# Kernel tuning notes

Measured on AMD Instinct MI355X. Metric: run time of the kernel, lower is better.

The kernel has to match this reference:

```python
import jax, jax.numpy as jnp
import numpy as np

N = 50000      # nodes
E = 800000     # edges
F = 32         # num_features (per-irrep channels, L=1 -> scalar + vector parts)
NINV = 128     # num_inv_features
NL = 4         # num_layers
H = 64         # edge-MLP hidden width (mlp_params)
G = 2048       # number of graphs
EPS = 1e-6


def setup_inputs() -> dict:
    key = jax.random.key(0)
    ks = jax.random.split(key, 24)
    inp = {
        "x": jax.random.normal(ks[0], (N, 5), jnp.float32),
        "pos": jax.random.normal(ks[1], (N, 3), jnp.float32),
        "edge_index": jax.random.randint(ks[2], (2, E), 0, N, jnp.int64),
        "edge_attr": jax.random.uniform(ks[3], (E, 4), jnp.float32),
        "batch": jnp.sort(jax.random.randint(ks[4], (N,), 0, G, jnp.int64)),
        # embedding block params (scalar and vector branches)
        "W_es": jax.random.normal(ks[5], (5, F), jnp.float32) * 0.3,
        "b_es": jnp.zeros((F,), jnp.float32),
        "W_ev": jax.random.normal(ks[6], (5, F), jnp.float32) * 0.3,
        # per-layer message-passing params, stacked over layers
        "W1": jax.random.normal(ks[7], (NL, 5, H), jnp.float32) * 0.3,
        "b1": jnp.zeros((NL, H), jnp.float32),
        "W2": jax.random.normal(ks[8], (NL, H, 3 * F), jnp.float32) * 0.1,
        "b2": jnp.zeros((NL, 3 * F), jnp.float32),
        "Ws": jax.random.normal(ks[9], (NL, F, F), jnp.float32) * 0.1,
        "Wv": jax.random.normal(ks[10], (NL, F, F), jnp.float32) * 0.1,
        # invariant map
        "W_inv": jax.random.normal(ks[11], (2 * F, NINV), jnp.float32) * 0.1,
        "b_inv": jnp.zeros((NINV,), jnp.float32),
        # fc head: BN -> ELU -> Linear -> BN -> ELU -> Linear(->1)
        "g1": jnp.ones((NINV,), jnp.float32),
        "be1": jnp.zeros((NINV,), jnp.float32),
        "Wf1": jax.random.normal(ks[12], (NINV, NINV), jnp.float32) * 0.1,
        "bf1": jnp.zeros((NINV,), jnp.float32),
        "g2": jnp.ones((NINV,), jnp.float32),
        "be2": jnp.zeros((NINV,), jnp.float32),
        "Wf2": jax.random.normal(ks[13], (NINV, 1), jnp.float32) * 0.1,
        "bf2": jnp.zeros((1,), jnp.float32),
    }
    return inp


def _bn(z, g, b):
    m = z.mean(0)
    va = z.var(0)
    return (z - m) * jax.lax.rsqrt(va + 1e-5) * g + b


def reference(x, pos, edge_index, edge_attr, batch,
              W_es, b_es, W_ev, W1, b1, W2, b2, Ws, Wv,
              W_inv, b_inv, g1, be1, Wf1, bf1, g2, be2, Wf2, bf2):
    src, dst = edge_index[0], edge_index[1]
    delta = pos[dst] - pos[src]                       # [E,3]
    d = jnp.sqrt(jnp.sum(delta * delta, -1) + EPS)    # [E]
    u = delta / d[:, None]                            # unit edge direction

    # embedding: L=1 steerable features = scalar [N,F] + vector [N,F,3]
    s = x @ W_es + b_es
    v = (x @ W_ev)[:, :, None] * pos[:, None, :]

    edge_in = jnp.concatenate([d[:, None], edge_attr], -1)   # [E,5]
    counts = jax.ops.segment_sum(jnp.ones((E,), s.dtype), dst, num_segments=N)
    denom = jnp.maximum(counts, 1.0)[:, None]

    for l in range(NL):  # residual message-passing blocks
        h = jax.nn.elu(edge_in @ W1[l] + b1[l]) @ W2[l] + b2[l]  # [E,3F]
        gs, gv, gsv = jnp.split(h, 3, axis=-1)
        ms = gs * s[src]                                          # [E,F]
        mv = gv[:, :, None] * v[src] + (gsv * s[src])[:, :, None] * u[:, None, :]  # [E,F,3]
        as_ = jax.ops.segment_sum(ms, dst, num_segments=N) / denom
        av = jax.ops.segment_sum(mv, dst, num_segments=N) / denom[:, :, None]
        s = s + jax.nn.elu(as_ @ Ws[l])
        v = v + jnp.einsum('nfd,fg->ngd', av, Wv[l])

    # invariant map: scalars + vector norms
    inv_feats = jnp.concatenate([s, jnp.sqrt(jnp.sum(v * v, -1) + EPS)], -1)
    inv = inv_feats @ W_inv + b_inv                               # [N,NINV]

    # global mean pool over graphs
    gcnt = jnp.maximum(jax.ops.segment_sum(jnp.ones((N,), inv.dtype), batch, num_segments=G), 1.0)[:, None]
    xg = jax.ops.segment_sum(inv, batch, num_segments=G) / gcnt   # [G,NINV]

    z = jax.nn.elu(_bn(xg, g1, be1)) @ Wf1 + bf1
    z = jax.nn.elu(_bn(z, g2, be2)) @ Wf2 + bf2                   # [G,1]
    return z
```

## Files before the change

kernel.cpp:

```cpp
#include <hip/hip_runtime.h>
#include <hip/hip_bf16.h>
#include <math.h>

#define NN 50000
#define EE 800000
#define FF 32
#define HH 64
#define GG 2048
#define NLAYERS 4
#define EPSF 1e-6f
#define TILES 4

typedef __attribute__((ext_vector_type(8))) short short8;
typedef __attribute__((ext_vector_type(4))) float f32x4;

__device__ __forceinline__ float elu_f(float x){ return x > 0.0f ? x : __expf(x) - 1.0f; }
__device__ __forceinline__ short f2bf_s(float x){
    __hip_bfloat16 h = __float2bfloat16(x);
    return *reinterpret_cast<short*>(&h);
}
__device__ __forceinline__ float bf2f(unsigned short u){
    unsigned int w = ((unsigned int)u) << 16;
    return *reinterpret_cast<float*>(&w);
}

__global__ __launch_bounds__(256) void k_count(const int* __restrict__ ei, int* __restrict__ counts)
{
    int e = blockIdx.x*256 + threadIdx.x;
    if (e >= EE) return;
    atomicAdd(&counts[ei[EE+e]], 1);
}

__global__ __launch_bounds__(1024) void k_scan(const int* __restrict__ counts, int* __restrict__ rowptr)
{
    __shared__ int sh[1024];
    const int CH = (NN + 1023)/1024;
    int t = threadIdx.x;
    int start = t*CH;
    int end = min(start+CH, NN);
    int s = 0;
    for (int i=start; i<end; i++) s += counts[i];
    sh[t] = s; __syncthreads();
    for (int off=1; off<1024; off<<=1){
        int v = (t>=off) ? sh[t-off] : 0;
        __syncthreads();
        sh[t] += v;
        __syncthreads();
    }
    int run = sh[t] - s;
    for (int i=start; i<end; i++){ rowptr[i] = run; run += counts[i]; }
    if (t==1023) rowptr[NN] = run;
}

__global__ __launch_bounds__(256) void k_fill(
    const int* __restrict__ ei, const float* __restrict__ pos, const float* __restrict__ eattr,
    const int* __restrict__ rowptr, int* __restrict__ cursor,
    int* __restrict__ esrc, float* __restrict__ ein8)
{
    int e = blockIdx.x*256 + threadIdx.x;
    if (e >= EE) return;
    int src = ei[e], dst = ei[EE+e];
    float dx = pos[dst*3+0]-pos[src*3+0];
    float dy = pos[dst*3+1]-pos[src*3+1];
    float dz = pos[dst*3+2]-pos[src*3+2];
    float d = sqrtf(dx*dx+dy*dy+dz*dz+EPSF);
    float inv = 1.0f/d;
    int slot = rowptr[dst] + atomicAdd(&cursor[dst], 1);
    esrc[slot] = src;
    float4* p = (float4*)(ein8 + (size_t)slot*8);
    p[0] = make_float4(d, eattr[e*4+0], eattr[e*4+1], eattr[e*4+2]);
    p[1] = make_float4(eattr[e*4+3], dx*inv, dy*inv, dz*inv);
}

__global__ __launch_bounds__(256) void k_embed(
    const float* __restrict__ x, const float* __restrict__ pos,
    const float* __restrict__ W_es, const float* __restrict__ b_es,
    const float* __restrict__ W_ev,
    float* __restrict__ ns, float* __restrict__ nv, __hip_bfloat16* __restrict__ nbf)
{
    int tid = blockIdx.x*256 + threadIdx.x;
    if (tid >= NN*FF) return;
    int n = tid >> 5, f = tid & 31;
    float x0=x[n*5+0], x1=x[n*5+1], x2=x[n*5+2], x3=x[n*5+3], x4=x[n*5+4];
    float s  = b_es[f] + x0*W_es[f] + x1*W_es[32+f] + x2*W_es[64+f] + x3*W_es[96+f] + x4*W_es[128+f];
    float vm =           x0*W_ev[f] + x1*W_ev[32+f] + x2*W_ev[64+f] + x3*W_ev[96+f] + x4*W_ev[128+f];
    float v0 = vm*pos[n*3+0], v1 = vm*pos[n*3+1], v2 = vm*pos[n*3+2];
    ns[tid] = s;
    nv[n*96+f*3+0] = v0;
    nv[n*96+f*3+1] = v1;
    nv[n*96+f*3+2] = v2;
    nbf[n*128+f] = __float2bfloat16(s);
    nbf[n*128+32+f*3+0] = __float2bfloat16(v0);
    nbf[n*128+32+f*3+1] = __float2bfloat16(v1);
    nbf[n*128+32+f*3+2] = __float2bfloat16(v2);
}

__global__ __launch_bounds__(256) void k_transpose(const float* __restrict__ W2, __hip_bfloat16* __restrict__ W2bf)
{
    int tid = blockIdx.x*256 + threadIdx.x;
    if (tid >= NLAYERS*6144) return;
    int l = tid / 6144; int r = tid - l*6144;
    int j = r >> 6; int k = r & 63;
    W2bf[l*6144 + j*64 + k] = __float2bfloat16(W2[l*6144 + k*96 + j]);
}

__global__ __launch_bounds__(256) void k_mlp_mfma(
    const float* __restrict__ ein8,
    const float* __restrict__ W1l, const float* __restrict__ b1l,
    const __hip_bfloat16* __restrict__ W2bfl, const float* __restrict__ b2l,
    __hip_bfloat16* __restrict__ hbuf)
{
    __shared__ __hip_bfloat16 cstage[2][64][100];
    const int tid  = threadIdx.x;
    const int lane = tid & 63;
    const int wave = tid >> 6;
    const int m    = lane & 15;
    const int quad = lane >> 4;

    for (int t=0; t<TILES; t++){
        const long long blockbase = ((long long)blockIdx.x*TILES + t) * 64;
        const long long edge = blockbase + wave*16 + m;

        const float4* p = (const float4*)(ein8 + edge*8);
        float4 q0 = p[0], q1 = p[1];
        float e0=q0.x, e1=q0.y, e2=q0.z, e3=q0.w, e4=q1.x;

        short8 afrag[2];
        #pragma unroll
        for (int s=0;s<2;s++){
            #pragma unroll
            for (int j=0;j<8;j++){
                int k = s*32 + quad*8 + j;
                float a = b1l[k] + e0*W1l[k] + e1*W1l[64+k] + e2*W1l[128+k]
                                 + e3*W1l[192+k] + e4*W1l[256+k];
                afrag[s][j] = f2bf_s(elu_f(a));
            }
        }

        f32x4 acc[6];
        #pragma unroll
        for (int u=0;u<6;u++) acc[u] = (f32x4){0.f,0.f,0.f,0.f};

        #pragma unroll
        for (int s=0;s<2;s++){
            #pragma unroll
            for (int u=0;u<6;u++){
                int n = u*16 + m;
                short8 bfrag = *(const short8*)(W2bfl + n*64 + s*32 + quad*8);
                acc[u] = __builtin_amdgcn_mfma_f32_16x16x32_bf16(afrag[s], bfrag, acc[u], 0, 0, 0);
            }
        }

        __hip_bfloat16 (*cs)[100] = cstage[t&1];
        #pragma unroll
        for (int u=0;u<6;u++){
            int n = u*16 + m;
            float bias = b2l[n];
            #pragma unroll
            for (int r=0;r<4;r++){
                cs[wave*16 + quad*4 + r][n] = __float2bfloat16(acc[u][r] + bias);
            }
        }
        __syncthreads();

        #pragma unroll
        for (int it=0; it<6; it++){
            int flat = it*256 + tid;
            int e = flat / 24, seg = flat % 24;
            float2 val = *(const float2*)&cs[e][seg*4];
            *(float2*)(hbuf + (blockbase + e)*96 + seg*4) = val;
        }
    }
}

__global__ __launch_bounds__(256) void k_agg(
    const int* __restrict__ rowptr, const int* __restrict__ esrc,
    const float* __restrict__ ein8, const __hip_bfloat16* __restrict__ hbuf,
    float* __restrict__ ns, float* __restrict__ nv,
    const __hip_bfloat16* __restrict__ nbfi,
    const float* __restrict__ Wsl, const float* __restrict__ Wvl,
    __hip_bfloat16* __restrict__ nbfo)
{
    int tid = blockIdx.x*256 + threadIdx.x;
    int n = tid >> 5, f = tid & 31;
    if (n >= NN) return;
    int beg = rowptr[n], end = rowptr[n+1];
    float as=0.f, a0=0.f, a1=0.f, a2=0.f;
    if (beg < end){
        const unsigned short* hb = (const unsigned short*)hbuf;
        const unsigned short* nb = (const unsigned short*)nbfi;
        int src = esrc[beg];
        float4 u = *(const float4*)(ein8 + (size_t)beg*8 + 4);
        size_t hoff = (size_t)beg*96;
        unsigned short hx = hb[hoff+f], hy = hb[hoff+32+f], hz = hb[hoff+64+f];
        size_t noff = (size_t)src*128;
        unsigned short sb = nb[noff+f];
        unsigned short vx = nb[noff+32+f*3+0], vy = nb[noff+32+f*3+1], vz = nb[noff+32+f*3+2];
        for (int slot=beg; slot<end; slot++){
            int srcN=0; float4 uN=u;
            unsigned short hxN=0,hyN=0,hzN=0,sbN=0,vxN=0,vyN=0,vzN=0;
            if (slot+1 < end){
                srcN = esrc[slot+1];
                uN = *(const float4*)(ein8 + (size_t)(slot+1)*8 + 4);
                size_t ho = (size_t)(slot+1)*96;
                hxN = hb[ho+f]; hyN = hb[ho+32+f]; hzN = hb[ho+64+f];
                size_t no = (size_t)srcN*128;
                sbN = nb[no+f];
                vxN = nb[no+32+f*3+0]; vyN = nb[no+32+f*3+1]; vzN = nb[no+32+f*3+2];
            }
            float gs = bf2f(hx), gv = bf2f(hy), gsv = bf2f(hz);
            float s  = bf2f(sb);
            float v0 = bf2f(vx), v1 = bf2f(vy), v2 = bf2f(vz);
            float c = gsv*s;
            as += gs*s;
            a0 += gv*v0 + c*u.y;
            a1 += gv*v1 + c*u.z;
            a2 += gv*v2 + c*u.w;
            src=srcN; u=uN; hx=hxN; hy=hyN; hz=hzN; sb=sbN; vx=vxN; vy=vyN; vz=vzN;
        }
    }
    float inv = 1.f/fmaxf((float)(end-beg), 1.f);
    as*=inv; a0*=inv; a1*=inv; a2*=inv;
    float os=0.f, o0=0.f, o1=0.f, o2=0.f;
    #pragma unroll
    for (int k=0;k<FF;k++){
        float bs = __shfl(as, k, 32);
        float b0 = __shfl(a0, k, 32);
        float b1 = __shfl(a1, k, 32);
        float b2 = __shfl(a2, k, 32);
        float ws = Wsl[k*32+f];
        float wv = Wvl[k*32+f];
        os += bs*ws; o0 += b0*wv; o1 += b1*wv; o2 += b2*wv;
    }
    float sn = ns[n*32+f] + elu_f(os);
    float w0 = nv[n*96+f*3+0] + o0;
    float w1 = nv[n*96+f*3+1] + o1;
    float w2 = nv[n*96+f*3+2] + o2;
    ns[n*32+f] = sn;
    nv[n*96+f*3+0] = w0;
    nv[n*96+f*3+1] = w1;
    nv[n*96+f*3+2] = w2;
    nbfo[n*128+f] = __float2bfloat16(sn);
    nbfo[n*128+32+f*3+0] = __float2bfloat16(w0);
    nbfo[n*128+32+f*3+1] = __float2bfloat16(w1);
    nbfo[n*128+32+f*3+2] = __float2bfloat16(w2);
}

__global__ __launch_bounds__(256) void k_gbounds(const int* __restrict__ batch, int* __restrict__ gstart)
{
    int g = blockIdx.x*256 + threadIdx.x;
    if (g > GG) return;
    int lo = 0, hi = NN;
    while (lo < hi){
        int mid = (lo+hi) >> 1;
        if (batch[mid] < g) lo = mid+1; else hi = mid;
    }
    gstart[g] = lo;
}

__global__ __launch_bounds__(128) void k_gpool(
    const int* __restrict__ gstart,
    const float* __restrict__ ns, const float* __restrict__ nv,
    const float* __restrict__ W_inv, const float* __restrict__ b_inv,
    float* __restrict__ xg)
{
    __shared__ float Wsh[64*128];
    __shared__ float feat[64];
    int g = blockIdx.x, j = threadIdx.x;
    for (int idx=j; idx<64*128; idx+=128) Wsh[idx] = W_inv[idx];
    int beg = gstart[g], end = gstart[g+1];
    float acc = 0.f;
    for (int n=beg; n<end; n++){
        __syncthreads();
        if (j < 32){
            feat[j] = ns[n*32+j];
        } else if (j < 64){
            int f = j-32;
            float v0=nv[n*96+f*3+0], v1=nv[n*96+f*3+1], v2=nv[n*96+f*3+2];
            feat[j] = sqrtf(v0*v0+v1*v1+v2*v2+EPSF);
        }
        __syncthreads();
        float a = 0.f;
        #pragma unroll
        for (int k=0;k<64;k++) a += feat[k]*Wsh[k*128+j];
        acc += a;
    }
    int cnt = end - beg;
    float cp = fmaxf((float)cnt, 1.f);
    xg[g*128+j] = acc/cp + b_inv[j]*((float)cnt/cp);
}

__global__ __launch_bounds__(256) void k_colstats(
    const float* __restrict__ in, float* __restrict__ mean, float* __restrict__ rstd)
{
    int j = blockIdx.x;
    float s=0.f, q=0.f;
    for (int g=threadIdx.x; g<GG; g+=256){
        float x = in[g*128+j];
        s += x; q += x*x;
    }
    __shared__ float rs[256], rq[256];
    rs[threadIdx.x]=s; rq[threadIdx.x]=q;
    __syncthreads();
    for (int st=128; st>0; st>>=1){
        if (threadIdx.x < st){ rs[threadIdx.x]+=rs[threadIdx.x+st]; rq[threadIdx.x]+=rq[threadIdx.x+st]; }
        __syncthreads();
    }
    if (threadIdx.x==0){
        float m = rs[0]/(float)GG;
        float v = rq[0]/(float)GG - m*m;
        mean[j]=m; rstd[j]=rsqrtf(v+1e-5f);
    }
}

__global__ __launch_bounds__(128) void k_fc1(
    const float* __restrict__ xg, const float* __restrict__ mean, const float* __restrict__ rstd,
    const float* __restrict__ g1, const float* __restrict__ be1,
    const float* __restrict__ Wf1, const float* __restrict__ bf1,
    float* __restrict__ z1)
{
    int g = blockIdx.x, j = threadIdx.x;
    __shared__ float a[128];
    float xin = xg[g*128+j];
    a[j] = elu_f((xin-mean[j])*rstd[j]*g1[j]+be1[j]);
    __syncthreads();
    float z = bf1[j];
    #pragma unroll 8
    for (int k=0;k<128;k++) z += a[k]*Wf1[k*128+j];
    z1[g*128+j] = z;
}

__global__ __launch_bounds__(128) void k_out(
    const float* __restrict__ z1, const float* __restrict__ mean, const float* __restrict__ rstd,
    const float* __restrict__ g2, const float* __restrict__ be2,
    const float* __restrict__ Wf2, const float* __restrict__ bf2,
    float* __restrict__ out)
{
    int g = blockIdx.x, j = threadIdx.x;
    float a = elu_f((z1[g*128+j]-mean[j])*rstd[j]*g2[j]+be2[j]) * Wf2[j];
    __shared__ float red[128];
    red[j]=a; __syncthreads();
    for (int st=64; st>0; st>>=1){
        if (j<st) red[j]+=red[j+st];
        __syncthreads();
    }
    if (j==0) out[g] = red[0] + bf2[0];
}

extern "C" void kernel_launch(void* const* d_in, const int* in_sizes, int n_in,
                              void* d_out, int out_size, void* d_ws, size_t ws_size,
                              hipStream_t stream)
{
    const float* x      = (const float*)d_in[0];
    const float* pos    = (const float*)d_in[1];
    const int*   ei     = (const int*)d_in[2];
    const float* eattr  = (const float*)d_in[3];
    const int*   batch  = (const int*)d_in[4];
    const float* W_es   = (const float*)d_in[5];
    const float* b_es   = (const float*)d_in[6];
    const float* W_ev   = (const float*)d_in[7];
    const float* W1     = (const float*)d_in[8];
    const float* b1     = (const float*)d_in[9];
    const float* W2     = (const float*)d_in[10];
    const float* b2     = (const float*)d_in[11];
    const float* Ws     = (const float*)d_in[12];
    const float* Wv     = (const float*)d_in[13];
    const float* W_inv  = (const float*)d_in[14];
    const float* b_inv  = (const float*)d_in[15];
    const float* g1     = (const float*)d_in[16];
    const float* be1    = (const float*)d_in[17];
    const float* Wf1    = (const float*)d_in[18];
    const float* bf1    = (const float*)d_in[19];
    const float* g2     = (const float*)d_in[20];
    const float* be2    = (const float*)d_in[21];
    const float* Wf2    = (const float*)d_in[22];
    const float* bf2    = (const float*)d_in[23];
    float* out = (float*)d_out;

    char* base = (char*)d_ws;
    size_t off = 0;
    auto alloc = [&](size_t elems4) {
        void* p = base + off;
        off += ((elems4*4 + 63) & ~size_t(63));
        return p;
    };
    int*   counts = (int*)  alloc(50000);
    int*   cursor = (int*)  alloc(50000);
    size_t zero_bytes = off;
    int*   rowptr = (int*)  alloc(50001);
    int*   esrc   = (int*)  alloc(800000);
    float* ein8   = (float*)alloc(6400000);
    float* ns     = (float*)alloc(1600000);
    float* nv     = (float*)alloc(4800000);
    __hip_bfloat16* nbfA = (__hip_bfloat16*)alloc(3200000);
    __hip_bfloat16* nbfB = (__hip_bfloat16*)alloc(3200000);
    __hip_bfloat16* W2bf = (__hip_bfloat16*)alloc(12288);
    int*   gstart = (int*)  alloc(2049);
    float* xg     = (float*)alloc(262144);
    float* z1     = (float*)alloc(262144);
    float* m1     = (float*)alloc(128);
    float* r1     = (float*)alloc(128);
    float* m2     = (float*)alloc(128);
    float* r2     = (float*)alloc(128);
    __hip_bfloat16* hbuf = (__hip_bfloat16*)alloc(38400000);

    hipMemsetAsync(d_ws, 0, zero_bytes, stream);

    k_count    <<<EE/256, 256, 0, stream>>>(ei, counts);
    k_scan     <<<1, 1024, 0, stream>>>(counts, rowptr);
    k_fill     <<<EE/256, 256, 0, stream>>>(ei, pos, eattr, rowptr, cursor, esrc, ein8);
    k_embed    <<<NN*FF/256, 256, 0, stream>>>(x, pos, W_es, b_es, W_ev, ns, nv, nbfA);
    k_transpose<<<(NLAYERS*6144+255)/256, 256, 0, stream>>>(W2, W2bf);

    for (int l=0; l<NLAYERS; l++){
        const __hip_bfloat16* nbfi = (l&1) ? nbfB : nbfA;
        __hip_bfloat16* nbfo = (l&1) ? nbfA : nbfB;
        k_mlp_mfma<<<EE/(64*TILES), 256, 0, stream>>>(ein8,
            W1 + l*320, b1 + l*64, W2bf + l*6144, b2 + l*96, hbuf);
        k_agg<<<(NN*32+255)/256, 256, 0, stream>>>(rowptr, esrc, ein8, hbuf,
            ns, nv, nbfi, Ws + l*1024, Wv + l*1024, nbfo);
    }

    k_gbounds <<<(GG+1+255)/256, 256, 0, stream>>>(batch, gstart);
    k_gpool   <<<GG, 128, 0, stream>>>(gstart, ns, nv, W_inv, b_inv, xg);
    k_colstats<<<128, 256, 0, stream>>>(xg, m1, r1);
    k_fc1     <<<GG, 128, 0, stream>>>(xg, m1, r1, g1, be1, Wf1, bf1, z1);
    k_colstats<<<128, 256, 0, stream>>>(z1, m2, r2);
    k_out     <<<GG, 128, 0, stream>>>(z1, m2, r2, g2, be2, Wf2, bf2, out);
}
```

Measured before the change: 1.005 ms.

## Interleave bf16 node features, split edges across half-waves, MFMA invariant map

```diff
diff --git a/kernel.cpp b/kernel.cpp
--- a/kernel.cpp
+++ b/kernel.cpp
@@ -13,6 +13,7 @@
 
 typedef __attribute__((ext_vector_type(8))) short short8;
 typedef __attribute__((ext_vector_type(4))) float f32x4;
+typedef __attribute__((ext_vector_type(4))) unsigned short us4;
 
 __device__ __forceinline__ float elu_f(float x){ return x > 0.0f ? x : __expf(x) - 1.0f; }
 __device__ __forceinline__ short f2bf_s(float x){
@@ -89,10 +90,12 @@
     nv[n*96+f*3+0] = v0;
     nv[n*96+f*3+1] = v1;
     nv[n*96+f*3+2] = v2;
-    nbf[n*128+f] = __float2bfloat16(s);
-    nbf[n*128+32+f*3+0] = __float2bfloat16(v0);
-    nbf[n*128+32+f*3+1] = __float2bfloat16(v1);
-    nbf[n*128+32+f*3+2] = __float2bfloat16(v2);
+    us4 q;
+    q[0] = (unsigned short)f2bf_s(s);
+    q[1] = (unsigned short)f2bf_s(v0);
+    q[2] = (unsigned short)f2bf_s(v1);
+    q[3] = (unsigned short)f2bf_s(v2);
+    *(us4*)((unsigned short*)nbf + (size_t)n*128 + f*4) = q;
 }
 
 __global__ __launch_bounds__(256) void k_transpose(const float* __restrict__ W2, __hip_bfloat16* __restrict__ W2bf)
@@ -102,6 +105,14 @@
     int l = tid / 6144; int r = tid - l*6144;
     int j = r >> 6; int k = r & 63;
     W2bf[l*6144 + j*64 + k] = __float2bfloat16(W2[l*6144 + k*96 + j]);
+}
+
+__global__ __launch_bounds__(256) void k_transposeW(const float* __restrict__ W_inv, __hip_bfloat16* __restrict__ WinvT)
+{
+    int tid = blockIdx.x*256 + threadIdx.x;
+    if (tid >= 8192) return;
+    int n = tid >> 6, k = tid & 63;
+    WinvT[n*64 + k] = __float2bfloat16(W_inv[k*128 + n]);
 }
 
 __global__ __launch_bounds__(256) void k_mlp_mfma(
@@ -182,45 +193,51 @@
     __hip_bfloat16* __restrict__ nbfo)
 {
     int tid = blockIdx.x*256 + threadIdx.x;
-    int n = tid >> 5, f = tid & 31;
+    int n = tid >> 6;
     if (n >= NN) return;
+    int lane = threadIdx.x & 63;
+    int f = lane & 31, h2 = lane >> 5;
     int beg = rowptr[n], end = rowptr[n+1];
     float as=0.f, a0=0.f, a1=0.f, a2=0.f;
-    if (beg < end){
+    {
         const unsigned short* hb = (const unsigned short*)hbuf;
         const unsigned short* nb = (const unsigned short*)nbfi;
-        int src = esrc[beg];
-        float4 u = *(const float4*)(ein8 + (size_t)beg*8 + 4);
-        size_t hoff = (size_t)beg*96;
-        unsigned short hx = hb[hoff+f], hy = hb[hoff+32+f], hz = hb[hoff+64+f];
-        size_t noff = (size_t)src*128;
-        unsigned short sb = nb[noff+f];
-        unsigned short vx = nb[noff+32+f*3+0], vy = nb[noff+32+f*3+1], vz = nb[noff+32+f*3+2];
-        for (int slot=beg; slot<end; slot++){
-            int srcN=0; float4 uN=u;
-            unsigned short hxN=0,hyN=0,hzN=0,sbN=0,vxN=0,vyN=0,vzN=0;
-            if (slot+1 < end){
-                srcN = esrc[slot+1];
-                uN = *(const float4*)(ein8 + (size_t)(slot+1)*8 + 4);
-                size_t ho = (size_t)(slot+1)*96;
-                hxN = hb[ho+f]; hyN = hb[ho+32+f]; hzN = hb[ho+64+f];
-                size_t no = (size_t)srcN*128;
-                sbN = nb[no+f];
-                vxN = nb[no+32+f*3+0]; vyN = nb[no+32+f*3+1]; vzN = nb[no+32+f*3+2];
+        int slot = beg + h2;
+        if (slot < end){
+            int src = esrc[slot];
+            float4 u = *(const float4*)(ein8 + (size_t)slot*8 + 4);
+            size_t ho = (size_t)slot*96;
+            unsigned short hx=hb[ho+f], hy=hb[ho+32+f], hz=hb[ho+64+f];
+            us4 nq = *(const us4*)(nb + (size_t)src*128 + f*4);
+            while (true){
+                int slot2 = slot + 2;
+                float4 uN=u; unsigned short hxN=0,hyN=0,hzN=0; us4 nqN=nq;
+                if (slot2 < end){
+                    int srcN = esrc[slot2];
+                    uN = *(const float4*)(ein8 + (size_t)slot2*8 + 4);
+                    size_t ho2 = (size_t)slot2*96;
+                    hxN=hb[ho2+f]; hyN=hb[ho2+32+f]; hzN=hb[ho2+64+f];
+                    nqN = *(const us4*)(nb + (size_t)srcN*128 + f*4);
+                }
+                float gs=bf2f(hx), gv=bf2f(hy), gsv=bf2f(hz);
+                float s  = bf2f(nq[0]);
+                float v0 = bf2f(nq[1]), v1 = bf2f(nq[2]), v2 = bf2f(nq[3]);
+                float c = gsv*s;
+                as += gs*s;
+                a0 += gv*v0 + c*u.y;
+                a1 += gv*v1 + c*u.z;
+                a2 += gv*v2 + c*u.w;
+                if (slot2 >= end) break;
+                slot = slot2; u=uN; hx=hxN; hy=hyN; hz=hzN; nq=nqN;
             }
-            float gs = bf2f(hx), gv = bf2f(hy), gsv = bf2f(hz);
-            float s  = bf2f(sb);
-            float v0 = bf2f(vx), v1 = bf2f(vy), v2 = bf2f(vz);
-            float c = gsv*s;
-            as += gs*s;
-            a0 += gv*v0 + c*u.y;
-            a1 += gv*v1 + c*u.z;
-            a2 += gv*v2 + c*u.w;
-            src=srcN; u=uN; hx=hxN; hy=hyN; hz=hzN; sb=sbN; vx=vxN; vy=vyN; vz=vzN;
-        }
-    }
-    float inv = 1.f/fmaxf((float)(end-beg), 1.f);
-    as*=inv; a0*=inv; a1*=inv; a2*=inv;
+        }
+    }
+    as += __shfl_xor(as, 32);
+    a0 += __shfl_xor(a0, 32);
+    a1 += __shfl_xor(a1, 32);
+    a2 += __shfl_xor(a2, 32);
+    float invd = 1.f/fmaxf((float)(end-beg), 1.f);
+    as*=invd; a0*=invd; a1*=invd; a2*=invd;
     float os=0.f, o0=0.f, o1=0.f, o2=0.f;
     #pragma unroll
     for (int k=0;k<FF;k++){
@@ -232,18 +249,22 @@
         float wv = Wvl[k*32+f];
         os += bs*ws; o0 += b0*wv; o1 += b1*wv; o2 += b2*wv;
     }
-    float sn = ns[n*32+f] + elu_f(os);
-    float w0 = nv[n*96+f*3+0] + o0;
-    float w1 = nv[n*96+f*3+1] + o1;
-    float w2 = nv[n*96+f*3+2] + o2;
-    ns[n*32+f] = sn;
-    nv[n*96+f*3+0] = w0;
-    nv[n*96+f*3+1] = w1;
-    nv[n*96+f*3+2] = w2;
-    nbfo[n*128+f] = __float2bfloat16(sn);
-    nbfo[n*128+32+f*3+0] = __float2bfloat16(w0);
-    nbfo[n*128+32+f*3+1] = __float2bfloat16(w1);
-    nbfo[n*128+32+f*3+2] = __float2bfloat16(w2);
+    if (h2 == 0){
+        float sn = ns[n*32+f] + elu_f(os);
+        float w0 = nv[n*96+f*3+0] + o0;
+        float w1 = nv[n*96+f*3+1] + o1;
+        float w2 = nv[n*96+f*3+2] + o2;
+        ns[n*32+f] = sn;
+        nv[n*96+f*3+0] = w0;
+        nv[n*96+f*3+1] = w1;
+        nv[n*96+f*3+2] = w2;
+        us4 q;
+        q[0] = (unsigned short)f2bf_s(sn);
+        q[1] = (unsigned short)f2bf_s(w0);
+        q[2] = (unsigned short)f2bf_s(w1);
+        q[3] = (unsigned short)f2bf_s(w2);
+        *(us4*)((unsigned short*)nbfo + (size_t)n*128 + f*4) = q;
+    }
 }
 
 __global__ __launch_bounds__(256) void k_gbounds(const int* __restrict__ batch, int* __restrict__ gstart)
@@ -258,33 +279,62 @@
     gstart[g] = lo;
 }
 
-__global__ __launch_bounds__(128) void k_gpool(
-    const int* __restrict__ gstart,
+__global__ __launch_bounds__(256) void k_invgemm(
     const float* __restrict__ ns, const float* __restrict__ nv,
-    const float* __restrict__ W_inv, const float* __restrict__ b_inv,
-    float* __restrict__ xg)
-{
-    __shared__ float Wsh[64*128];
-    __shared__ float feat[64];
+    const __hip_bfloat16* __restrict__ WinvT,
+    float* __restrict__ inv)
+{
+    const int tid  = threadIdx.x;
+    const int lane = tid & 63;
+    const int wave = tid >> 6;
+    const int m    = lane & 15;
+    const int quad = lane >> 4;
+    const int tilebase = blockIdx.x*64 + wave*16;
+    const int node = tilebase + m;
+    const bool valid = node < NN;
+
+    short8 afrag[2];
+    #pragma unroll
+    for (int j=0;j<8;j++){
+        int k = quad*8 + j;
+        float fs = valid ? ns[(size_t)node*32 + k] : 0.f;
+        afrag[0][j] = f2bf_s(fs);
+        float v0 = valid ? nv[(size_t)node*96 + k*3+0] : 0.f;
+        float v1 = valid ? nv[(size_t)node*96 + k*3+1] : 0.f;
+        float v2 = valid ? nv[(size_t)node*96 + k*3+2] : 0.f;
+        afrag[1][j] = f2bf_s(sqrtf(v0*v0+v1*v1+v2*v2+EPSF));
+    }
+    f32x4 acc[8];
+    #pragma unroll
+    for (int t=0;t<8;t++) acc[t] = (f32x4){0.f,0.f,0.f,0.f};
+    #pragma unroll
+    for (int s=0;s<2;s++){
+        #pragma unroll
+        for (int t=0;t<8;t++){
+            short8 bfrag = *(const short8*)(WinvT + (t*16+m)*64 + s*32 + quad*8);
+            acc[t] = __builtin_amdgcn_mfma_f32_16x16x32_bf16(afrag[s], bfrag, acc[t], 0, 0, 0);
+        }
+    }
+    #pragma unroll
+    for (int r=0;r<4;r++){
+        int nrow = tilebase + quad*4 + r;
+        if (nrow < NN){
+            #pragma unroll
+            for (int t=0;t<8;t++){
+                inv[(size_t)nrow*128 + t*16 + m] = acc[t][r];
+            }
+        }
+    }
+}
+
+__global__ __launch_bounds__(128) void k_pool(
+    const int* __restrict__ gstart, const float* __restrict__ inv,
+    const float* __restrict__ b_inv, float* __restrict__ xg)
+{
     int g = blockIdx.x, j = threadIdx.x;
-    for (int idx=j; idx<64*128; idx+=128) Wsh[idx] = W_inv[idx];
     int beg = gstart[g], end = gstart[g+1];
     float acc = 0.f;
-    for (int n=beg; n<end; n++){
-        __syncthreads();
-        if (j < 32){
-            feat[j] = ns[n*32+j];
-        } else if (j < 64){
-            int f = j-32;
-            float v0=nv[n*96+f*3+0], v1=nv[n*96+f*3+1], v2=nv[n*96+f*3+2];
-            feat[j] = sqrtf(v0*v0+v1*v1+v2*v2+EPSF);
-        }
-        __syncthreads();
-        float a = 0.f;
-        #pragma unroll
-        for (int k=0;k<64;k++) a += feat[k]*Wsh[k*128+j];
-        acc += a;
-    }
+    for (int n=beg; n<end; n++) acc += inv[(size_t)n*128 + j];
     int cnt = end - beg;
     float cp = fmaxf((float)cnt, 1.f);
     xg[g*128+j] = acc/cp + b_inv[j]*((float)cnt/cp);
@@ -395,6 +445,7 @@
     __hip_bfloat16* nbfA = (__hip_bfloat16*)alloc(3200000);
     __hip_bfloat16* nbfB = (__hip_bfloat16*)alloc(3200000);
     __hip_bfloat16* W2bf = (__hip_bfloat16*)alloc(12288);
+    __hip_bfloat16* WinvT= (__hip_bfloat16*)alloc(4096);
     int*   gstart = (int*)  alloc(2049);
     float* xg     = (float*)alloc(262144);
     float* z1     = (float*)alloc(262144);
@@ -403,6 +454,7 @@
     float* m2     = (float*)alloc(128);
     float* r2     = (float*)alloc(128);
     __hip_bfloat16* hbuf = (__hip_bfloat16*)alloc(38400000);
+    float* inv    = (float*)hbuf;
 
     hipMemsetAsync(d_ws, 0, zero_bytes, stream);
 
@@ -411,18 +463,20 @@
     k_fill     <<<EE/256, 256, 0, stream>>>(ei, pos, eattr, rowptr, cursor, esrc, ein8);
     k_embed    <<<NN*FF/256, 256, 0, stream>>>(x, pos, W_es, b_es, W_ev, ns, nv, nbfA);
     k_transpose<<<(NLAYERS*6144+255)/256, 256, 0, stream>>>(W2, W2bf);
+    k_transposeW<<<(8192+255)/256, 256, 0, stream>>>(W_inv, WinvT);
 
     for (int l=0; l<NLAYERS; l++){
         const __hip_bfloat16* nbfi = (l&1) ? nbfB : nbfA;
         __hip_bfloat16* nbfo = (l&1) ? nbfA : nbfB;
         k_mlp_mfma<<<EE/(64*TILES), 256, 0, stream>>>(ein8,
             W1 + l*320, b1 + l*64, W2bf + l*6144, b2 + l*96, hbuf);
-        k_agg<<<(NN*32+255)/256, 256, 0, stream>>>(rowptr, esrc, ein8, hbuf,
+        k_agg<<<(NN*64+255)/256, 256, 0, stream>>>(rowptr, esrc, ein8, hbuf,
             ns, nv, nbfi, Ws + l*1024, Wv + l*1024, nbfo);
     }
 
     k_gbounds <<<(GG+1+255)/256, 256, 0, stream>>>(batch, gstart);
-    k_gpool   <<<GG, 128, 0, stream>>>(gstart, ns, nv, W_inv, b_inv, xg);
+    k_invgemm <<<(NN+63)/64, 256, 0, stream>>>(ns, nv, WinvT, inv);
+    k_pool    <<<GG, 128, 0, stream>>>(gstart, inv, b_inv, xg);
     k_colstats<<<128, 256, 0, stream>>>(xg, m1, r1);
     k_fc1     <<<GG, 128, 0, stream>>>(xg, m1, r1, g1, be1, Wf1, bf1, z1);
     k_colstats<<<128, 256, 0, stream>>>(z1, m2, r2);
```

Result: slower. 1.251 ms (+24.4%).
